# Optimization experiments

Hardware: AMD Instinct MI355X
Metric: run time of the kernel (lower is better)

## Reference

```python
import jax, jax.numpy as jnp
import numpy as np

TOP_K = 2
N_EXPERTS = 8

def setup_inputs() -> dict:
    key = jax.random.key(0)
    k1, k2, k3, k4 = jax.random.split(key, 4)
    B, C, L, O, E = 8, 4096, 1024, 1024, N_EXPERTS
    scale = 1.0 / np.sqrt(L)
    return {
        "x": jax.random.normal(k1, (B, C, L), dtype=jnp.float32),
        "gate_w": jax.random.normal(k2, (E, L), dtype=jnp.float32) * scale,
        "expert_w": jax.random.normal(k3, (E, O, L), dtype=jnp.float32) * scale,
        "expert_b": jax.random.normal(k4, (E, O), dtype=jnp.float32) * scale,
    }

def reference(x, gate_w, expert_w, expert_b):
    B, C, L = x.shape
    E, O, _ = expert_w.shape
    xt = x.reshape(-1, L)                                  # [T, L], T = B*C
    router_logits = jnp.einsum('tl,el->te', xt, gate_w)    # [T, E]
    probs = jax.nn.softmax(router_logits.astype(jnp.float32), axis=-1)
    routing_weights, selected = jax.lax.top_k(probs, TOP_K)  # [T, K] each
    # combine weight per (token, expert): sum of top-k weights routed to that expert
    comb = jnp.sum(jax.nn.one_hot(selected, E, dtype=routing_weights.dtype)
                   * routing_weights[..., None], axis=1)   # [T, E]
    comb = comb.astype(x.dtype)
    out = jnp.zeros((xt.shape[0], O), dtype=x.dtype)
    for e in range(E):  # small fixed expert loop; masked dense combine
        ye = xt @ expert_w[e].T + expert_b[e]              # [T, O]
        out = out + ye * comb[:, e:e + 1]
    return out.reshape(B, C, O)
```

## Files before the change

### kernel.cpp

```cpp
#include <hip/hip_runtime.h>
#include <cstdint>
#include <cstddef>

#define E_EXP 8
#define LDIM 1024
#define ODIM 1024
#define NPAIR 64

#define BM 256
#define BN 128
#define BK 32
#define NKT (LDIM / BK)
#define MAXRT 160
#define GEMM_GRID (MAXRT * 8)
#define CPX (GEMM_GRID / 8)

typedef __bf16 bf16x8 __attribute__((ext_vector_type(8)));
typedef float f32x4 __attribute__((ext_vector_type(4)));

__device__ __forceinline__ unsigned short f2bf(float f) {
  uint32_t u = __float_as_uint(f);
  u += 0x7FFFu + ((u >> 16) & 1u);
  return (unsigned short)(u >> 16);
}

__device__ __forceinline__ void gload_lds16(const void* g, void* l) {
  __builtin_amdgcn_global_load_lds(
      (const __attribute__((address_space(1))) unsigned int*)g,
      (__attribute__((address_space(3))) unsigned int*)l, 16, 0, 0);
}

__global__ __launch_bounds__(256) void route_kernel(
    const float* __restrict__ x, const float* __restrict__ gate,
    unsigned short* __restrict__ xb, int* __restrict__ sel,
    float2* __restrict__ pw, int T)
{
  const int wid = threadIdx.x >> 6, lane = threadIdx.x & 63;
  const int tok = blockIdx.x * 4 + wid;
  if (tok >= T) return;
  const float* xr = x + (size_t)tok * LDIM;
  unsigned short* xbr = xb + (size_t)tok * LDIM;

  float acc[E_EXP];
#pragma unroll
  for (int e = 0; e < E_EXP; ++e) acc[e] = 0.f;

#pragma unroll
  for (int it = 0; it < 4; ++it) {
    const int c = it * 256 + lane * 4;
    float4 xv = *(const float4*)(xr + c);
    ushort4 bvv;
    bvv.x = f2bf(xv.x); bvv.y = f2bf(xv.y); bvv.z = f2bf(xv.z); bvv.w = f2bf(xv.w);
    *(ushort4*)(xbr + c) = bvv;
#pragma unroll
    for (int e = 0; e < E_EXP; ++e) {
      float4 gv = *(const float4*)(gate + e * LDIM + c);
      acc[e] += xv.x * gv.x + xv.y * gv.y + xv.z * gv.z + xv.w * gv.w;
    }
  }
#pragma unroll
  for (int off = 32; off >= 1; off >>= 1) {
#pragma unroll
    for (int e = 0; e < E_EXP; ++e) acc[e] += __shfl_xor(acc[e], off, 64);
  }
  if (lane == 0) {
    int i1 = 0; float m1 = acc[0];
#pragma unroll
    for (int e = 1; e < E_EXP; ++e) if (acc[e] > m1) { m1 = acc[e]; i1 = e; }
    int i2 = -1; float m2 = -1e30f;
#pragma unroll
    for (int e = 0; e < E_EXP; ++e) if (e != i1 && acc[e] > m2) { m2 = acc[e]; i2 = e; }
    float s = 0.f;
#pragma unroll
    for (int e = 0; e < E_EXP; ++e) s += __expf(acc[e] - m1);
    const float inv = 1.f / s;
    sel[tok] = i1 | (i2 << 4);
    pw[tok] = make_float2(inv, __expf(m2 - m1) * inv);
  }
}

__global__ __launch_bounds__(256) void hist_kernel(
    const int* __restrict__ sel, int* __restrict__ hist2d, int T)
{
  __shared__ int h[NPAIR];
  const int tid = threadIdx.x;
  if (tid < NPAIR) h[tid] = 0;
  __syncthreads();
  const int t0 = blockIdx.x * 2048;
#pragma unroll
  for (int i = 0; i < 8; ++i) {
    const int t = t0 + i * 256 + tid;
    if (t < T) {
      const int s = sel[t];
      const int i1 = s & 15, i2 = (s >> 4) & 15;
      const int lo = i1 < i2 ? i1 : i2, hi = i1 < i2 ? i2 : i1;
      atomicAdd(&h[lo * 8 + hi], 1);
    }
  }
  __syncthreads();
  if (tid < NPAIR) hist2d[blockIdx.x * NPAIR + tid] = h[tid];
}

__global__ void finalize_kernel(
    const int* __restrict__ hist2d, int nb,
    int* __restrict__ blockBase, int4* __restrict__ desc, int* __restrict__ meta)
{
  __shared__ int pcnt[NPAIR], pbase[NPAIR];
  const int p = threadIdx.x;
  if (p < NPAIR) {
    int c = 0;
#pragma unroll 4
    for (int b = 0; b < nb; ++b) c += hist2d[b * NPAIR + p];
    pcnt[p] = c;
  }
  __syncthreads();
  if (p == 0) {
    int s = 0;
    for (int q = 0; q < NPAIR; ++q) { pbase[q] = s; s += pcnt[q]; }
  }
  __syncthreads();
  if (p < NPAIR) {
    int run = pbase[p];
    for (int b = 0; b < nb; ++b) {
      blockBase[b * NPAIR + p] = run;
      run += hist2d[b * NPAIR + p];
    }
  }
  if (p == 0) {
    int rt = 0;
    for (int q = 0; q < NPAIR; ++q) {
      const int lo = q >> 3, hi = q & 7;
      for (int j = 0; j * BM < pcnt[q]; ++j) {
        int rows = pcnt[q] - j * BM; if (rows > BM) rows = BM;
        desc[rt] = make_int4(lo | (hi << 8), pbase[q] + j * BM, rows, 0);
        ++rt;
      }
    }
    meta[0] = rt;
  }
}

__global__ __launch_bounds__(256) void scatter_kernel(
    const int* __restrict__ sel, const float2* __restrict__ pw,
    const int* __restrict__ blockBase, int* __restrict__ tokC,
    float2* __restrict__ wC, int T)
{
  __shared__ int cur[NPAIR];
  const int tid = threadIdx.x;
  if (tid < NPAIR) cur[tid] = blockBase[blockIdx.x * NPAIR + tid];
  __syncthreads();
  const int t0 = blockIdx.x * 2048;
#pragma unroll
  for (int i = 0; i < 8; ++i) {
    const int t = t0 + i * 256 + tid;
    if (t < T) {
      const int s = sel[t];
      const int i1 = s & 15, i2 = (s >> 4) & 15;
      const float2 w = pw[t];
      const int lo = i1 < i2 ? i1 : i2, hi = i1 < i2 ? i2 : i1;
      const float wlo = i1 < i2 ? w.x : w.y;
      const float whi = i1 < i2 ? w.y : w.x;
      const int pos = atomicAdd(&cur[lo * 8 + hi], 1);
      tokC[pos] = t;
      wC[pos] = make_float2(wlo, whi);
    }
  }
}

__global__ __launch_bounds__(256) void convw_kernel(
    const float* __restrict__ w, unsigned short* __restrict__ wb, int n4)
{
  int i = blockIdx.x * 256 + threadIdx.x;
  if (i >= n4) return;
  float4 v = *(const float4*)(w + (size_t)i * 4);
  ushort4 b;
  b.x = f2bf(v.x); b.y = f2bf(v.y); b.z = f2bf(v.z); b.w = f2bf(v.w);
  *(ushort4*)(wb + (size_t)i * 4) = b;
}

__global__ __launch_bounds__(512, 2) void moe_gemm_pair(
    const unsigned short* __restrict__ xb, const unsigned short* __restrict__ wb,
    const float* __restrict__ bias, const int4* __restrict__ desc,
    const int* __restrict__ meta, const int* __restrict__ tokC,
    const float2* __restrict__ wC, float* __restrict__ out)
{
  __shared__ __align__(16) unsigned short ldsA[4][BM * BK];
  __shared__ __align__(16) unsigned short ldsB[4][2 * BN * BK];
  const int tid = threadIdx.x;
  const int lane = tid & 63, w = tid >> 6;
  const int wm = w >> 2, wn = w & 3;

  const int totalRT = meta[0];
  const int swz = ((int)blockIdx.x & 7) * CPX + ((int)blockIdx.x >> 3);
  if (swz >= totalRT * 8) return;
  const int rt = swz >> 3, colTile = swz & 7;
  const int4 d = desc[rt];
  const int lo = d.x & 255, hi = d.x >> 8;
  const int start = d.y, ce = d.z;
  const int* tokL = tokC + start;
  const float2* wgtL = wC + start;

  const int s = lane & 3;
  const int rA0 = w * 32 + (lane >> 2);
  const int rA1 = rA0 + 16;
  const int gA0 = s ^ ((rA0 >> 1) & 3);
  const int gA1 = s ^ ((rA1 >> 1) & 3);
  const int tA0 = tokL[rA0 < ce ? rA0 : ce - 1];
  const int tA1 = tokL[rA1 < ce ? rA1 : ce - 1];
  const char* aSrc0 = (const char*)(xb + (size_t)tA0 * LDIM) + gA0 * 16;
  const char* aSrc1 = (const char*)(xb + (size_t)tA1 * LDIM) + gA1 * 16;
  const int rB = w * 16 + (lane >> 2);
  const int gB = s ^ ((rB >> 1) & 3);
  const int colB = colTile * BN + rB;
  const char* bSrcLo = (const char*)(wb + ((size_t)lo * ODIM + colB) * LDIM) + gB * 16;
  const char* bSrcHi = (const char*)(wb + ((size_t)hi * ODIM + colB) * LDIM) + gB * 16;

  int offA[8], offB[2];
#pragma unroll
  for (int fr = 0; fr < 8; ++fr) {
    const int r = wm * 128 + fr * 16 + (lane & 15);
    offA[fr] = r * BK + (((lane >> 4) ^ ((r >> 1) & 3)) * 8);
  }
#pragma unroll
  for (int fc = 0; fc < 2; ++fc) {
    const int r = wn * 32 + fc * 16 + (lane & 15);
    offB[fc] = r * BK + (((lane >> 4) ^ ((r >> 1) & 3)) * 8);
  }

  auto stage = [&](int b, int kt) {
    const int kb = kt * 64;
    gload_lds16(aSrc0 + kb, &ldsA[b][w * 1024]);
    gload_lds16(aSrc1 + kb, &ldsA[b][w * 1024 + 512]);
    gload_lds16(bSrcLo + kb, &ldsB[b][w * 512]);
    gload_lds16(bSrcHi + kb, &ldsB[b][4096 + w * 512]);
  };

  auto readFrags = [&](int b, bf16x8 (&af)[8], bf16x8 (&bl)[2], bf16x8 (&bh)[2]) {
    const unsigned short* As = &ldsA[b][0];
    const unsigned short* Bs = &ldsB[b][0];
#pragma unroll
    for (int fr = 0; fr < 8; ++fr) af[fr] = *(const bf16x8*)(As + offA[fr]);
#pragma unroll
    for (int fc = 0; fc < 2; ++fc) {
      bl[fc] = *(const bf16x8*)(Bs + offB[fc]);
      bh[fc] = *(const bf16x8*)(Bs + 4096 + offB[fc]);
    }
  };

  f32x4 acc[2][8][2] = {};

  auto mfmaCl = [&](bf16x8 (&af)[8], bf16x8 (&bl)[2], bf16x8 (&bh)[2]) {
#pragma unroll
    for (int fr = 0; fr < 8; ++fr) {
      acc[0][fr][0] = __builtin_amdgcn_mfma_f32_16x16x32_bf16(af[fr], bl[0], acc[0][fr][0], 0, 0, 0);
      acc[0][fr][1] = __builtin_amdgcn_mfma_f32_16x16x32_bf16(af[fr], bl[1], acc[0][fr][1], 0, 0, 0);
      acc[1][fr][0] = __builtin_amdgcn_mfma_f32_16x16x32_bf16(af[fr], bh[0], acc[1][fr][0], 0, 0, 0);
      acc[1][fr][1] = __builtin_amdgcn_mfma_f32_16x16x32_bf16(af[fr], bh[1], acc[1][fr][1], 0, 0, 0);
    }
  };

  bf16x8 afA[8], blA[2], bhA[2], afB[8], blB[2], bhB[2];

  stage(0, 0); stage(1, 1); stage(2, 2); stage(3, 3);
  asm volatile("s_waitcnt vmcnt(8)" ::: "memory");
  __builtin_amdgcn_s_barrier();
  readFrags(0, afA, blA, bhA);
  asm volatile("s_waitcnt lgkmcnt(0)" ::: "memory");
  __builtin_amdgcn_s_barrier();

#define GEMM_BODY(T_, AFc, BLc, BHc, AFn, BLn, BHn)                          \
  {                                                                          \
    stage((T_) & 3, (T_) + 4 < NKT ? (T_) + 4 : NKT - 1);                    \
    if ((T_) + 1 < NKT) readFrags(((T_) + 1) & 3, AFn, BLn, BHn);            \
    __builtin_amdgcn_s_setprio(1);                                           \
    mfmaCl(AFc, BLc, BHc);                                                   \
    __builtin_amdgcn_s_setprio(0);                                           \
    asm volatile("s_waitcnt lgkmcnt(0)" ::: "memory");                       \
    asm volatile("s_waitcnt vmcnt(8)" ::: "memory");                         \
    __builtin_amdgcn_s_barrier();                                            \
  }

#pragma unroll 1
  for (int t2 = 0; t2 < NKT; t2 += 2) {
    GEMM_BODY(t2,     afA, blA, bhA, afB, blB, bhB);
    GEMM_BODY(t2 + 1, afB, blB, bhB, afA, blA, bhA);
  }
#undef GEMM_BODY

  int cols[2]; float bLo[2], bHi[2];
#pragma unroll
  for (int fc = 0; fc < 2; ++fc) {
    cols[fc] = colTile * BN + wn * 32 + fc * 16 + (lane & 15);
    bLo[fc] = bias[lo * ODIM + cols[fc]];
    bHi[fc] = bias[hi * ODIM + cols[fc]];
  }
#pragma unroll
  for (int fr = 0; fr < 8; ++fr) {
#pragma unroll
    for (int rr = 0; rr < 4; ++rr) {
      const int row = wm * 128 + fr * 16 + (lane >> 4) * 4 + rr;
      if (row < ce) {
        const int tok = tokL[row];
        const float2 ww = wgtL[row];
        float* orow = out + (size_t)tok * ODIM;
#pragma unroll
        for (int fc = 0; fc < 2; ++fc)
          orow[cols[fc]] = ww.x * (acc[0][fr][fc][rr] + bLo[fc]) +
                           ww.y * (acc[1][fr][fc][rr] + bHi[fc]);
      }
    }
  }
}

__global__ __launch_bounds__(256) void naive_moe(
    const float* __restrict__ x, const float* __restrict__ gate,
    const float* __restrict__ ew, const float* __restrict__ eb,
    float* __restrict__ out, int T)
{
  const int tok = blockIdx.x, tid = threadIdx.x;
  __shared__ float xs[LDIM];
  __shared__ float logits[E_EXP];
  __shared__ float sw1, sw2; __shared__ int si1, si2;
  for (int i = tid; i < LDIM; i += 256) xs[i] = x[(size_t)tok * LDIM + i];
  __syncthreads();
  const int wid = tid >> 6, lane = tid & 63;
  for (int e = wid; e < E_EXP; e += 4) {
    float a = 0.f;
    for (int i = lane; i < LDIM; i += 64) a += xs[i] * gate[e * LDIM + i];
    for (int off = 32; off >= 1; off >>= 1) a += __shfl_xor(a, off, 64);
    if (lane == 0) logits[e] = a;
  }
  __syncthreads();
  if (tid == 0) {
    int i1 = 0; float m1 = logits[0];
    for (int e = 1; e < E_EXP; ++e) if (logits[e] > m1) { m1 = logits[e]; i1 = e; }
    int i2 = -1; float m2 = -1e30f;
    for (int e = 0; e < E_EXP; ++e) if (e != i1 && logits[e] > m2) { m2 = logits[e]; i2 = e; }
    float s = 0.f;
    for (int e = 0; e < E_EXP; ++e) s += __expf(logits[e] - m1);
    si1 = i1; si2 = i2; sw1 = 1.f / s; sw2 = __expf(m2 - m1) / s;
  }
  __syncthreads();
  const int i1 = si1, i2 = si2; const float w1 = sw1, w2 = sw2;
  for (int o = tid; o < ODIM; o += 256) {
    float a1 = 0.f, a2 = 0.f;
    const float* p1 = ew + ((size_t)i1 * ODIM + o) * LDIM;
    const float* p2 = ew + ((size_t)i2 * ODIM + o) * LDIM;
    for (int l = 0; l < LDIM; ++l) { a1 += xs[l] * p1[l]; a2 += xs[l] * p2[l]; }
    out[(size_t)tok * ODIM + o] =
        w1 * (a1 + eb[i1 * ODIM + o]) + w2 * (a2 + eb[i2 * ODIM + o]);
  }
}

extern "C" void kernel_launch(void* const* d_in, const int* in_sizes, int n_in,
                              void* d_out, int out_size, void* d_ws, size_t ws_size,
                              hipStream_t stream) {
  const float* x    = (const float*)d_in[0];
  const float* gate = (const float*)d_in[1];
  const float* ew   = (const float*)d_in[2];
  const float* eb   = (const float*)d_in[3];
  float* out = (float*)d_out;
  const int T = in_sizes[0] / LDIM;
  const int NB = (T + 2047) / 2048;

  const size_t offSel   = 0;
  const size_t offPw    = offSel + (size_t)T * 4;
  const size_t offHist  = offPw + (size_t)T * 8;
  const size_t offBBase = offHist + (size_t)NB * NPAIR * 4;
  const size_t offDesc  = offBBase + (size_t)NB * NPAIR * 4;
  const size_t offMeta  = offDesc + (size_t)MAXRT * 16;
  const size_t offTokC  = offMeta + 256;
  const size_t offWC    = offTokC + (size_t)T * 4;
  const size_t offXb    = offWC + (size_t)T * 8;
  const size_t offWb    = offXb + (size_t)T * LDIM * 2;
  const size_t need     = offWb + (size_t)E_EXP * ODIM * LDIM * 2;

  if (ws_size < need) {
    naive_moe<<<T, 256, 0, stream>>>(x, gate, ew, eb, out, T);
    return;
  }

  char* ws = (char*)d_ws;

  route_kernel<<<(T + 3) / 4, 256, 0, stream>>>(
      x, gate, (unsigned short*)(ws + offXb), (int*)(ws + offSel),
      (float2*)(ws + offPw), T);

  const int n4 = E_EXP * ODIM * LDIM / 4;
  convw_kernel<<<(n4 + 255) / 256, 256, 0, stream>>>(ew, (unsigned short*)(ws + offWb), n4);

  hist_kernel<<<NB, 256, 0, stream>>>(
      (const int*)(ws + offSel), (int*)(ws + offHist), T);

  finalize_kernel<<<1, 64, 0, stream>>>(
      (const int*)(ws + offHist), NB, (int*)(ws + offBBase),
      (int4*)(ws + offDesc), (int*)(ws + offMeta));

  scatter_kernel<<<NB, 256, 0, stream>>>(
      (const int*)(ws + offSel), (const float2*)(ws + offPw),
      (const int*)(ws + offBBase), (int*)(ws + offTokC),
      (float2*)(ws + offWC), T);

  moe_gemm_pair<<<GEMM_GRID, 512, 0, stream>>>(
      (const unsigned short*)(ws + offXb), (const unsigned short*)(ws + offWb),
      eb, (const int4*)(ws + offDesc), (const int*)(ws + offMeta),
      (const int*)(ws + offTokC), (const float2*)(ws + offWC), out);
}
```

Baseline: 326.4 us.

## Load expert weights directly to registers and batch four tokens per router wave

The grouped GEMM no longer stages the weight (B) tiles through LDS. Each lane loads its bf16 weight fragments straight from global memory into registers one k-step ahead, and the A ring shrinks from four to three LDS buffers with a prefetch distance of two. This cuts LDS footprint and LDS traffic but makes weight reads uncoalesced per-lane 16-byte loads with less latency hiding. Separately, the router kernel now has each wave handle four tokens, reusing each gate vector load across them and launching a quarter as many blocks. The four-token loop has no per-token bound check, so it relies on T being a multiple of four.

```diff
diff --git a/kernel.cpp b/kernel.cpp
--- a/kernel.cpp
+++ b/kernel.cpp
@@ -36,46 +36,63 @@
     float2* __restrict__ pw, int T)
 {
   const int wid = threadIdx.x >> 6, lane = threadIdx.x & 63;
-  const int tok = blockIdx.x * 4 + wid;
-  if (tok >= T) return;
-  const float* xr = x + (size_t)tok * LDIM;
-  unsigned short* xbr = xb + (size_t)tok * LDIM;
-
-  float acc[E_EXP];
-#pragma unroll
-  for (int e = 0; e < E_EXP; ++e) acc[e] = 0.f;
+  const int tokBase = blockIdx.x * 16 + wid * 4;
+  if (tokBase >= T) return;
+  const float* xr = x + (size_t)tokBase * LDIM;
+  unsigned short* xbr = xb + (size_t)tokBase * LDIM;
+
+  float acc[4][E_EXP];
+#pragma unroll
+  for (int j = 0; j < 4; ++j)
+#pragma unroll
+    for (int e = 0; e < E_EXP; ++e) acc[j][e] = 0.f;
 
 #pragma unroll
   for (int it = 0; it < 4; ++it) {
     const int c = it * 256 + lane * 4;
-    float4 xv = *(const float4*)(xr + c);
-    ushort4 bvv;
-    bvv.x = f2bf(xv.x); bvv.y = f2bf(xv.y); bvv.z = f2bf(xv.z); bvv.w = f2bf(xv.w);
-    *(ushort4*)(xbr + c) = bvv;
+    float4 xv[4];
+#pragma unroll
+    for (int j = 0; j < 4; ++j) {
+      xv[j] = *(const float4*)(xr + (size_t)j * LDIM + c);
+      ushort4 bv;
+      bv.x = f2bf(xv[j].x); bv.y = f2bf(xv[j].y);
+      bv.z = f2bf(xv[j].z); bv.w = f2bf(xv[j].w);
+      *(ushort4*)(xbr + (size_t)j * LDIM + c) = bv;
+    }
 #pragma unroll
     for (int e = 0; e < E_EXP; ++e) {
       float4 gv = *(const float4*)(gate + e * LDIM + c);
-      acc[e] += xv.x * gv.x + xv.y * gv.y + xv.z * gv.z + xv.w * gv.w;
+#pragma unroll
+      for (int j = 0; j < 4; ++j)
+        acc[j][e] += xv[j].x * gv.x + xv[j].y * gv.y + xv[j].z * gv.z + xv[j].w * gv.w;
     }
   }
 #pragma unroll
   for (int off = 32; off >= 1; off >>= 1) {
 #pragma unroll
-    for (int e = 0; e < E_EXP; ++e) acc[e] += __shfl_xor(acc[e], off, 64);
-  }
-  if (lane == 0) {
-    int i1 = 0; float m1 = acc[0];
-#pragma unroll
-    for (int e = 1; e < E_EXP; ++e) if (acc[e] > m1) { m1 = acc[e]; i1 = e; }
-    int i2 = -1; float m2 = -1e30f;
-#pragma unroll
-    for (int e = 0; e < E_EXP; ++e) if (e != i1 && acc[e] > m2) { m2 = acc[e]; i2 = e; }
-    float s = 0.f;
-#pragma unroll
-    for (int e = 0; e < E_EXP; ++e) s += __expf(acc[e] - m1);
-    const float inv = 1.f / s;
-    sel[tok] = i1 | (i2 << 4);
-    pw[tok] = make_float2(inv, __expf(m2 - m1) * inv);
+    for (int j = 0; j < 4; ++j)
+#pragma unroll
+      for (int e = 0; e < E_EXP; ++e) acc[j][e] += __shfl_xor(acc[j][e], off, 64);
+  }
+  if (lane < 4) {
+    const int tok = tokBase + lane;
+    if (tok < T) {
+      float lg[E_EXP];
+#pragma unroll
+      for (int e = 0; e < E_EXP; ++e) lg[e] = acc[lane][e];
+      int i1 = 0; float m1 = lg[0];
+#pragma unroll
+      for (int e = 1; e < E_EXP; ++e) if (lg[e] > m1) { m1 = lg[e]; i1 = e; }
+      int i2 = -1; float m2 = -1e30f;
+#pragma unroll
+      for (int e = 0; e < E_EXP; ++e) if (e != i1 && lg[e] > m2) { m2 = lg[e]; i2 = e; }
+      float s = 0.f;
+#pragma unroll
+      for (int e = 0; e < E_EXP; ++e) s += __expf(lg[e] - m1);
+      const float inv = 1.f / s;
+      sel[tok] = i1 | (i2 << 4);
+      pw[tok] = make_float2(inv, __expf(m2 - m1) * inv);
+    }
   }
 }
 
@@ -184,8 +201,7 @@
     const int* __restrict__ meta, const int* __restrict__ tokC,
     const float2* __restrict__ wC, float* __restrict__ out)
 {
-  __shared__ __align__(16) unsigned short ldsA[4][BM * BK];
-  __shared__ __align__(16) unsigned short ldsB[4][2 * BN * BK];
+  __shared__ __align__(16) unsigned short ldsA[3][BM * BK];
   const int tid = threadIdx.x;
   const int lane = tid & 63, w = tid >> 6;
   const int wm = w >> 2, wn = w & 3;
@@ -209,42 +225,23 @@
   const int tA1 = tokL[rA1 < ce ? rA1 : ce - 1];
   const char* aSrc0 = (const char*)(xb + (size_t)tA0 * LDIM) + gA0 * 16;
   const char* aSrc1 = (const char*)(xb + (size_t)tA1 * LDIM) + gA1 * 16;
-  const int rB = w * 16 + (lane >> 2);
-  const int gB = s ^ ((rB >> 1) & 3);
-  const int colB = colTile * BN + rB;
-  const char* bSrcLo = (const char*)(wb + ((size_t)lo * ODIM + colB) * LDIM) + gB * 16;
-  const char* bSrcHi = (const char*)(wb + ((size_t)hi * ODIM + colB) * LDIM) + gB * 16;
-
-  int offA[8], offB[2];
+
+  const unsigned short* bPL =
+      wb + ((size_t)lo * ODIM + colTile * BN + wn * 32 + (lane & 15)) * LDIM + (lane >> 4) * 8;
+  const unsigned short* bPH =
+      wb + ((size_t)hi * ODIM + colTile * BN + wn * 32 + (lane & 15)) * LDIM + (lane >> 4) * 8;
+
+  int offA[8];
 #pragma unroll
   for (int fr = 0; fr < 8; ++fr) {
     const int r = wm * 128 + fr * 16 + (lane & 15);
     offA[fr] = r * BK + (((lane >> 4) ^ ((r >> 1) & 3)) * 8);
-  }
-#pragma unroll
-  for (int fc = 0; fc < 2; ++fc) {
-    const int r = wn * 32 + fc * 16 + (lane & 15);
-    offB[fc] = r * BK + (((lane >> 4) ^ ((r >> 1) & 3)) * 8);
   }
 
   auto stage = [&](int b, int kt) {
     const int kb = kt * 64;
     gload_lds16(aSrc0 + kb, &ldsA[b][w * 1024]);
     gload_lds16(aSrc1 + kb, &ldsA[b][w * 1024 + 512]);
-    gload_lds16(bSrcLo + kb, &ldsB[b][w * 512]);
-    gload_lds16(bSrcHi + kb, &ldsB[b][4096 + w * 512]);
-  };
-
-  auto readFrags = [&](int b, bf16x8 (&af)[8], bf16x8 (&bl)[2], bf16x8 (&bh)[2]) {
-    const unsigned short* As = &ldsA[b][0];
-    const unsigned short* Bs = &ldsB[b][0];
-#pragma unroll
-    for (int fr = 0; fr < 8; ++fr) af[fr] = *(const bf16x8*)(As + offA[fr]);
-#pragma unroll
-    for (int fc = 0; fc < 2; ++fc) {
-      bl[fc] = *(const bf16x8*)(Bs + offB[fc]);
-      bh[fc] = *(const bf16x8*)(Bs + 4096 + offB[fc]);
-    }
   };
 
   f32x4 acc[2][8][2] = {};
@@ -258,32 +255,43 @@
       acc[1][fr][1] = __builtin_amdgcn_mfma_f32_16x16x32_bf16(af[fr], bh[1], acc[1][fr][1], 0, 0, 0);
     }
   };
-
-  bf16x8 afA[8], blA[2], bhA[2], afB[8], blB[2], bhB[2];
-
-  stage(0, 0); stage(1, 1); stage(2, 2); stage(3, 3);
-  asm volatile("s_waitcnt vmcnt(8)" ::: "memory");
+  auto loadB = [&](int kt, bf16x8 (&bl)[2], bf16x8 (&bh)[2]) {
+    bl[0] = *(const bf16x8*)(bPL + kt * 32);
+    bl[1] = *(const bf16x8*)(bPL + 16 * LDIM + kt * 32);
+    bh[0] = *(const bf16x8*)(bPH + kt * 32);
+    bh[1] = *(const bf16x8*)(bPH + 16 * LDIM + kt * 32);
+  };
+
+  bf16x8 blA[2], bhA[2], blB[2], bhB[2];
+
+  stage(0, 0); stage(1, 1);
+  loadB(0, blA, bhA);
+  asm volatile("s_waitcnt vmcnt(6)" ::: "memory");
   __builtin_amdgcn_s_barrier();
-  readFrags(0, afA, blA, bhA);
-  asm volatile("s_waitcnt lgkmcnt(0)" ::: "memory");
-  __builtin_amdgcn_s_barrier();
-
-#define GEMM_BODY(T_, AFc, BLc, BHc, AFn, BLn, BHn)                          \
+
+  int buf = 0;
+#define GEMM_BODY(T_, BLc, BHc, BLn, BHn)                                    \
   {                                                                          \
-    stage((T_) & 3, (T_) + 4 < NKT ? (T_) + 4 : NKT - 1);                    \
-    if ((T_) + 1 < NKT) readFrags(((T_) + 1) & 3, AFn, BLn, BHn);            \
+    const unsigned short* As = &ldsA[buf][0];                                \
+    bf16x8 af[8];                                                            \
+    _Pragma("unroll")                                                        \
+    for (int fr = 0; fr < 8; ++fr) af[fr] = *(const bf16x8*)(As + offA[fr]); \
+    int sb = buf + 2; if (sb > 2) sb -= 3;                                   \
+    stage(sb, (T_) + 2 < NKT ? (T_) + 2 : NKT - 1);                          \
     __builtin_amdgcn_s_setprio(1);                                           \
-    mfmaCl(AFc, BLc, BHc);                                                   \
+    mfmaCl(af, BLc, BHc);                                                    \
     __builtin_amdgcn_s_setprio(0);                                           \
+    loadB((T_) + 1 < NKT ? (T_) + 1 : NKT - 1, BLn, BHn);                    \
     asm volatile("s_waitcnt lgkmcnt(0)" ::: "memory");                       \
-    asm volatile("s_waitcnt vmcnt(8)" ::: "memory");                         \
+    asm volatile("s_waitcnt vmcnt(6)" ::: "memory");                         \
     __builtin_amdgcn_s_barrier();                                            \
+    buf = (buf == 2) ? 0 : buf + 1;                                          \
   }
 
 #pragma unroll 1
   for (int t2 = 0; t2 < NKT; t2 += 2) {
-    GEMM_BODY(t2,     afA, blA, bhA, afB, blB, bhB);
-    GEMM_BODY(t2 + 1, afB, blB, bhB, afA, blA, bhA);
+    GEMM_BODY(t2,     blA, bhA, blB, bhB);
+    GEMM_BODY(t2 + 1, blB, bhB, blA, bhA);
   }
 #undef GEMM_BODY
 
@@ -382,7 +390,7 @@
 
   char* ws = (char*)d_ws;
 
-  route_kernel<<<(T + 3) / 4, 256, 0, stream>>>(
+  route_kernel<<<(T + 15) / 16, 256, 0, stream>>>(
       x, gate, (unsigned short*)(ws + offXb), (int*)(ws + offSel),
       (float2*)(ws + offPw), T);
 
```

Measured after the change: 348.5 us. 1.07x slower.
